# Kernel optimization log

Hardware: AMD Instinct MI355X
Metric: run time of the kernel (lower is better)

The kernel has to match this reference:

```python
import jax, jax.numpy as jnp
import numpy as np

B, A, H, DKEY, NMEM = 1024, 4, 512, 512, 65536
OBS, E1, E2 = 9, 64, 128
DIN = E2 + A + 1  # 133


def _lin_init(k, out_d, in_d):
    s = 1.0 / np.sqrt(in_d)
    kw, kb = jax.random.split(k)
    w = jax.random.uniform(kw, (out_d, in_d), jnp.float32, -s, s)
    b = jax.random.uniform(kb, (out_d,), jnp.float32, -s, s)
    return w, b


def setup_inputs() -> dict:
    key = jax.random.key(0)
    ks = jax.random.split(key, 16)
    inp = {}
    inp["obs"] = jax.random.normal(ks[0], (B, OBS), jnp.float32)
    inp["p_action"] = jax.random.uniform(ks[1], (B, A), jnp.float32)
    inp["p_reward"] = jax.random.normal(ks[2], (B, 1), jnp.float32)
    inp["h0"] = jnp.zeros((1, B, H), jnp.float32)
    inp["c0"] = jnp.zeros((1, B, H), jnp.float32)
    inp["cue"] = jax.random.normal(ks[3], (B, DKEY), jnp.float32)
    # encoder params
    inp["enc_w1"], inp["enc_b1"] = _lin_init(ks[4], E1, OBS)
    inp["enc_w2"], inp["enc_b2"] = _lin_init(ks[5], E2, E1)
    # episodic LSTM params (5 gates: i, f, g, o, r)
    s = 1.0 / np.sqrt(H)
    inp["w_ih"] = jax.random.uniform(ks[6], (5 * H, DIN), jnp.float32, -s, s)
    inp["w_hh"] = jax.random.uniform(ks[7], (5 * H, H), jnp.float32, -s, s)
    inp["b_ih"] = jax.random.uniform(ks[8], (5 * H,), jnp.float32, -s, s)
    inp["b_hh"] = jax.random.uniform(ks[9], (5 * H,), jnp.float32, -s, s)
    # actor / critic heads
    inp["actor_w"], inp["actor_b"] = _lin_init(ks[10], A, H)
    inp["critic_w"], inp["critic_b"] = _lin_init(ks[11], 1, H)
    # DND memory store (keys / values)
    inp["dnd_keys"] = jax.random.normal(ks[12], (NMEM, DKEY), jnp.float32)
    inp["dnd_vals"] = jax.random.normal(ks[13], (NMEM, H), jnp.float32) * 0.1
    return inp


def reference(obs, p_action, p_reward, h0, c0, cue,
              enc_w1, enc_b1, enc_w2, enc_b2,
              w_ih, w_hh, b_ih, b_hh,
              actor_w, actor_b, critic_w, critic_b,
              dnd_keys, dnd_vals):
    # --- encoder MLP ---
    feats = jax.nn.relu(jax.nn.relu(obs @ enc_w1.T + enc_b1) @ enc_w2.T + enc_b2)  # [B, 128]
    x_t = jnp.concatenate([feats, p_action, p_reward], axis=-1)  # [B, DIN]

    # --- DND retrieval: l2 kernel -> softmax-weighted sum of values ---
    d2 = (jnp.sum(cue * cue, axis=-1, keepdims=True)
          - 2.0 * (cue @ dnd_keys.T)
          + jnp.sum(dnd_keys * dnd_keys, axis=-1))  # [B, NMEM]
    sims = -jnp.sqrt(jnp.maximum(d2, 1e-12))
    w = jax.nn.softmax(sims, axis=-1)
    m_t = w @ dnd_vals  # [B, H]

    # --- episodic LSTM step (single timestep) ---
    h, c = h0[0], c0[0]  # [B, H]
    z = x_t @ w_ih.T + h @ w_hh.T + b_ih + b_hh  # [B, 5H]
    i_g = jax.nn.sigmoid(z[:, 0 * H:1 * H])
    f_g = jax.nn.sigmoid(z[:, 1 * H:2 * H])
    g_g = jnp.tanh(z[:, 2 * H:3 * H])
    o_g = jax.nn.sigmoid(z[:, 3 * H:4 * H])
    r_g = jax.nn.sigmoid(z[:, 4 * H:5 * H])  # reinstatement gate for memory
    c_new = f_g * c + i_g * g_g + r_g * m_t
    h_new = o_g * jnp.tanh(c_new)

    # --- heads ---
    action_logits = h_new @ actor_w.T + actor_b  # [B, A]
    value_estimate = h_new @ critic_w.T + critic_b  # [B, 1]
    return action_logits, value_estimate, h_new[None], c_new[None], feats
```

## Files before the change

### kernel.cpp

```cpp
#include <hip/hip_runtime.h>

typedef __bf16 bf16x8 __attribute__((ext_vector_type(8)));
typedef float  f32x4  __attribute__((ext_vector_type(4)));

#define NMEM_   65536
#define NCHUNK_ 16
#define NKC_    (NMEM_/NCHUNK_)
#define XPD_    160

#define WS_KB    ((size_t)0)
#define WS_VT    ((size_t)67108864)
#define WS_KNRM  ((size_t)134217728)
#define WS_QB    ((size_t)134479872)
#define WS_QQ    ((size_t)135528448)
#define WS_OP    ((size_t)135532544)
#define WS_LP    ((size_t)169086976)
#define WS_MT    ((size_t)169152512)
#define WS_XP    ((size_t)171249664)
#define WS_HB    ((size_t)171577344)
#define WS_WIHP  ((size_t)172625920)
#define WS_WHHB  ((size_t)173445120)
#define WS_Z     ((size_t)176066560)

#define OUT_LOG   0
#define OUT_VAL   4096
#define OUT_H     5120
#define OUT_C     529408
#define OUT_FEATS 1053696

__device__ __forceinline__ void gload16(const void* g, void* l) {
    __builtin_amdgcn_global_load_lds(
        (const __attribute__((address_space(1))) void*)g,
        (__attribute__((address_space(3))) void*)l, 16, 0, 0);
}

__global__ __launch_bounds__(256) void enc_kernel(
    const float* __restrict__ obs, const float* __restrict__ pa, const float* __restrict__ pr,
    const float* __restrict__ w1, const float* __restrict__ b1,
    const float* __restrict__ w2, const float* __restrict__ b2,
    float* __restrict__ feats_out, __bf16* __restrict__ xp)
{
    __shared__ float W1s[64*9];
    __shared__ float B1s[64];
    __shared__ float W2s[128*64];
    __shared__ float B2s[128];
    int t = threadIdx.x;
    for (int i = t; i < 64*9;   i += 256) W1s[i] = w1[i];
    for (int i = t; i < 64;     i += 256) B1s[i] = b1[i];
    for (int i = t; i < 128*64; i += 256) W2s[i] = w2[i];
    for (int i = t; i < 128;    i += 256) B2s[i] = b2[i];
    __syncthreads();
    int row = blockIdx.x * 256 + t;
    float ob[9];
    #pragma unroll
    for (int j = 0; j < 9; j++) ob[j] = obs[row*9 + j];
    float h1[64];
    #pragma unroll 4
    for (int i = 0; i < 64; i++) {
        float a = B1s[i];
        #pragma unroll
        for (int j = 0; j < 9; j++) a += ob[j] * W1s[i*9 + j];
        h1[i] = fmaxf(a, 0.f);
    }
    for (int j = 0; j < 128; j += 4) {
        float a0 = B2s[j], a1 = B2s[j+1], a2 = B2s[j+2], a3 = B2s[j+3];
        for (int i = 0; i < 64; i++) {
            float h = h1[i];
            a0 += h * W2s[(j+0)*64 + i];
            a1 += h * W2s[(j+1)*64 + i];
            a2 += h * W2s[(j+2)*64 + i];
            a3 += h * W2s[(j+3)*64 + i];
        }
        a0 = fmaxf(a0,0.f); a1 = fmaxf(a1,0.f); a2 = fmaxf(a2,0.f); a3 = fmaxf(a3,0.f);
        feats_out[row*128 + j+0] = a0; feats_out[row*128 + j+1] = a1;
        feats_out[row*128 + j+2] = a2; feats_out[row*128 + j+3] = a3;
        xp[row*XPD_ + j+0] = (__bf16)a0; xp[row*XPD_ + j+1] = (__bf16)a1;
        xp[row*XPD_ + j+2] = (__bf16)a2; xp[row*XPD_ + j+3] = (__bf16)a3;
    }
    #pragma unroll
    for (int k = 0; k < 4; k++) xp[row*XPD_ + 128 + k] = (__bf16)pa[row*4 + k];
    xp[row*XPD_ + 132] = (__bf16)pr[row];
    #pragma unroll
    for (int c = 133; c < 160; c++) xp[row*XPD_ + c] = (__bf16)0.f;
}

#define CV_KEYS 16384
#define CV_CUE  (CV_KEYS + 256)
#define CV_VT   (CV_CUE + 8192)
#define CM_N1 (2560*512)
#define CM_N2 (1024*512)
#define CM_N3 (2560*160)
#define CV_ALL  (CV_VT + (CM_N1 + CM_N2 + CM_N3 + 255)/256)

__global__ __launch_bounds__(256) void conv_all(
    const float* __restrict__ keys, const float* __restrict__ cue,
    const float* __restrict__ vals,
    const float* __restrict__ whh, const float* __restrict__ h0,
    const float* __restrict__ wih,
    __bf16* __restrict__ Kb, float* __restrict__ knrm,
    __bf16* __restrict__ Qb, float* __restrict__ qq,
    __bf16* __restrict__ Vt,
    __bf16* __restrict__ Whhb, __bf16* __restrict__ Hb, __bf16* __restrict__ Wihp)
{
    int bid = blockIdx.x;
    if (bid < CV_CUE) {
        const float* src; __bf16* dst; float* nrm; int swz, rbase;
        if (bid < CV_KEYS) { src = keys; dst = Kb; nrm = knrm; swz = 1; rbase = bid*4; }
        else               { src = cue;  dst = Qb; nrm = qq;  swz = 0; rbase = (bid-CV_KEYS)*4; }
        int row  = rbase + (threadIdx.x >> 6);
        int lane = threadIdx.x & 63;
        const float* s = src + (size_t)row * 512 + lane * 8;
        float4 v0 = *(const float4*)s;
        float4 v1 = *(const float4*)(s + 4);
        float ss = v0.x*v0.x + v0.y*v0.y + v0.z*v0.z + v0.w*v0.w
                 + v1.x*v1.x + v1.y*v1.y + v1.z*v1.z + v1.w*v1.w;
        bf16x8 o;
        o[0]=(__bf16)v0.x; o[1]=(__bf16)v0.y; o[2]=(__bf16)v0.z; o[3]=(__bf16)v0.w;
        o[4]=(__bf16)v1.x; o[5]=(__bf16)v1.y; o[6]=(__bf16)v1.z; o[7]=(__bf16)v1.w;
        int xorv = swz ? ((row & 15) << 4) : 0;
        *(bf16x8*)((char*)dst + (size_t)row * 1024 + ((lane * 16) ^ xorv)) = o;
        #pragma unroll
        for (int m = 1; m < 64; m <<= 1) ss += __shfl_xor(ss, m, 64);
        if (lane == 0) nrm[row] = ss;
        return;
    }
    if (bid < CV_VT) {
        __shared__ float Ls[64*65];
        int local = bid - CV_CUE;
        int k0 = (local & 1023) * 64, d0 = (local >> 10) * 64;
        int rr = threadIdx.x >> 6, cc = threadIdx.x & 63;
        #pragma unroll
        for (int i = 0; i < 16; i++) {
            int row = i*4 + rr;
            Ls[row*65 + cc] = vals[(size_t)(k0 + row) * 512 + d0 + cc];
        }
        __syncthreads();
        #pragma unroll
        for (int i = 0; i < 16; i++) {
            int drow = i*4 + rr;
            Vt[(size_t)(d0 + drow) * 65536 + k0 + cc] = (__bf16)Ls[cc*65 + drow];
        }
        return;
    }
    {
        int i = (bid - CV_VT) * 256 + threadIdx.x;
        if (i < CM_N1) { Whhb[i] = (__bf16)whh[i]; return; }
        i -= CM_N1;
        if (i < CM_N2) { Hb[i] = (__bf16)h0[i]; return; }
        i -= CM_N2;
        if (i < CM_N3) {
            int r = i / 160, c = i - r * 160;
            Wihp[i] = (c < 133) ? (__bf16)wih[r*133 + c] : (__bf16)0.f;
        }
    }
}

__global__ __launch_bounds__(512) void flash_kernel(
    const __bf16* __restrict__ Kb, const __bf16* __restrict__ Vt,
    const __bf16* __restrict__ Qb, const float* __restrict__ qq,
    const float* __restrict__ knrm,
    float* __restrict__ Opart, float* __restrict__ Lpart)
{
    extern __shared__ char smem[];
    char*   KL = smem;
    __bf16* Pl = (__bf16*)(smem + 131072);
    float*  Lb = (float*) (smem + 149504);

    const int tid = threadIdx.x, lane = tid & 63, w = tid >> 6;
    const int wq = w >> 1, wk = w & 1;
    const int lr = lane & 15, lq = lane >> 4;
    const int chunk = blockIdx.x & 15, qt = blockIdx.x >> 4;
    const int q0 = qt * 64, key0 = chunk * NKC_;

    bf16x8 qA[16];
    #pragma unroll
    for (int ks = 0; ks < 16; ks++)
        qA[ks] = *(const bf16x8*)(Qb + (size_t)(q0 + wq*16 + lr)*512 + ks*32 + lq*8);
    float qq4[4];
    #pragma unroll
    for (int r = 0; r < 4; r++)
        qq4[r] = qq[q0 + wq*16 + lq*4 + r];

    const float*  knp  = knrm + key0 + wk*32 + lr;
    const __bf16* vrow = Vt + (size_t)(w*64 + lr)*65536 + key0 + lq*8;
    const char*   kg   = (const char*)Kb + (size_t)key0 * 1024;

    #pragma unroll
    for (int r = 0; r < 8; ++r)
        gload16(kg + r*8192 + w*1024 + lane*16, KL + r*8192 + w*1024);
    asm volatile("s_waitcnt vmcnt(0)" ::: "memory");
    __builtin_amdgcn_s_barrier();

    f32x4 oacc[4][4] = {};
    float lsum[4] = {};
    int cur = 0;

    #pragma unroll 1
    for (int t = 0; t < 64; ++t) {
        float kn0 = knp[t*64];
        float kn1 = knp[t*64 + 16];
        const __bf16* vb = vrow + ((t + 63) & 63) * 64;
        bf16x8 vf[2][4];
        #pragma unroll
        for (int k2 = 0; k2 < 2; ++k2)
            #pragma unroll
            for (int mf = 0; mf < 4; ++mf)
                vf[k2][mf] = *(const bf16x8*)(vb + k2*32 + (size_t)mf*1048576);
        {
            const char* src = kg + (size_t)((t+1)&63)*65536;
            char* dst = KL + (cur^1)*65536;
            #pragma unroll
            for (int r = 0; r < 8; ++r)
                gload16(src + r*8192 + w*1024 + lane*16, dst + r*8192 + w*1024);
        }
        asm volatile("s_waitcnt vmcnt(18) lgkmcnt(0)" ::: "memory");
        __builtin_amdgcn_sched_barrier(0);
        __builtin_amdgcn_s_barrier();
        const char* kl = KL + cur*65536 + (wk*32 + lr)*1024;
        f32x4 s0 = {0.f,0.f,0.f,0.f}, s1 = {0.f,0.f,0.f,0.f};
        __builtin_amdgcn_s_setprio(1);
        #pragma unroll
        for (int ks = 0; ks < 16; ++ks) {
            int off = (ks*64 + lq*16) ^ (lr << 4);
            bf16x8 kf0 = *(const bf16x8*)(kl + off);
            bf16x8 kf1 = *(const bf16x8*)(kl + 16384 + off);
            s0 = __builtin_amdgcn_mfma_f32_16x16x32_bf16(qA[ks], kf0, s0, 0, 0, 0);
            s1 = __builtin_amdgcn_mfma_f32_16x16x32_bf16(qA[ks], kf1, s1, 0, 0, 0);
        }
        if (t) {
            const char* pr_ = (const char*)Pl + ((t+1)&1)*9216 + lr*144 + lq*16;
            #pragma unroll
            for (int k2 = 0; k2 < 2; ++k2)
                #pragma unroll
                for (int f2 = 0; f2 < 4; ++f2) {
                    bf16x8 pf = *(const bf16x8*)(pr_ + f2*2304 + k2*64);
                    #pragma unroll
                    for (int mf = 0; mf < 4; ++mf)
                        oacc[mf][f2] = __builtin_amdgcn_mfma_f32_16x16x32_bf16(
                            vf[k2][mf], pf, oacc[mf][f2], 0, 0, 0);
                }
        }
        __builtin_amdgcn_s_setprio(0);
        __bf16* Pw = Pl + (t&1)*4608 + wk*32 + lr;
        #pragma unroll
        for (int r = 0; r < 4; ++r) {
            float d20 = fmaxf(qq4[r] + kn0 - 2.f*s0[r], 1e-12f);
            float d21 = fmaxf(qq4[r] + kn1 - 2.f*s1[r], 1e-12f);
            float p0 = __expf(-__builtin_amdgcn_sqrtf(d20));
            float p1 = __expf(-__builtin_amdgcn_sqrtf(d21));
            lsum[r] += p0 + p1;
            Pw[(wq*16 + lq*4 + r)*72]      = (__bf16)p0;
            Pw[(wq*16 + lq*4 + r)*72 + 16] = (__bf16)p1;
        }
        cur ^= 1;
    }

    {
        const __bf16* vb = vrow + 63*64;
        bf16x8 vf[2][4];
        #pragma unroll
        for (int k2 = 0; k2 < 2; ++k2)
            #pragma unroll
            for (int mf = 0; mf < 4; ++mf)
                vf[k2][mf] = *(const bf16x8*)(vb + k2*32 + (size_t)mf*1048576);
        asm volatile("s_waitcnt lgkmcnt(0)" ::: "memory");
        __builtin_amdgcn_sched_barrier(0);
        __builtin_amdgcn_s_barrier();
        const char* pr_ = (const char*)Pl + 9216 + lr*144 + lq*16;
        #pragma unroll
        for (int k2 = 0; k2 < 2; ++k2)
            #pragma unroll
            for (int f2 = 0; f2 < 4; ++f2) {
                bf16x8 pf = *(const bf16x8*)(pr_ + f2*2304 + k2*64);
                #pragma unroll
                for (int mf = 0; mf < 4; ++mf)
                    oacc[mf][f2] = __builtin_amdgcn_mfma_f32_16x16x32_bf16(
                        vf[k2][mf], pf, oacc[mf][f2], 0, 0, 0);
            }
    }
    asm volatile("s_waitcnt vmcnt(0)" ::: "memory");

    const size_t obase = (size_t)((chunk*16 + qt)*512) * 64;
    #pragma unroll
    for (int mf = 0; mf < 4; ++mf)
        #pragma unroll
        for (int f2 = 0; f2 < 4; ++f2)
            #pragma unroll
            for (int r = 0; r < 4; ++r) {
                int d = w*64 + mf*16 + lq*4 + r;
                Opart[obase + (size_t)d*64 + f2*16 + lr] = oacc[mf][f2][r];
            }
    #pragma unroll
    for (int r = 0; r < 4; ++r) {
        float s = lsum[r];
        s += __shfl_xor(s, 1, 64); s += __shfl_xor(s, 2, 64);
        s += __shfl_xor(s, 4, 64); s += __shfl_xor(s, 8, 64);
        if (lr == 0) Lb[(wq*16 + lq*4 + r)*2 + wk] = s;
    }
    __syncthreads();
    if (tid < 64)
        Lpart[chunk*1024 + q0 + tid] = Lb[tid*2] + Lb[tid*2 + 1];
}

__global__ __launch_bounds__(256) void combine_kernel(
    const float* __restrict__ Opart, const float* __restrict__ Lpart,
    float* __restrict__ mt)
{
    __shared__ float Ts[64*65];
    __shared__ float Ls[64];
    int qt = blockIdx.x, db = blockIdx.y * 64, t = threadIdx.x;
    float acc[16] = {};
    for (int c = 0; c < NCHUNK_; c++) {
        size_t base = (size_t)((c*16 + qt)*512 + db) * 64;
        #pragma unroll
        for (int i = 0; i < 16; i++) acc[i] += Opart[base + t + 256*i];
    }
    if (t < 64) {
        float s = 0.f;
        for (int c = 0; c < NCHUNK_; c++) s += Lpart[c*1024 + qt*64 + t];
        Ls[t] = 1.f / s;
    }
    #pragma unroll
    for (int i = 0; i < 16; i++) {
        int idx = t + 256*i;
        Ts[(idx >> 6)*65 + (idx & 63)] = acc[i];
    }
    __syncthreads();
    #pragma unroll
    for (int i = 0; i < 16; i++) {
        int widx = t + 256*i;
        int dloc = widx & 63, ql = widx >> 6;
        mt[(size_t)(qt*64 + ql)*512 + db + dloc] = Ts[dloc*65 + ql] * Ls[ql];
    }
}

__global__ __launch_bounds__(256) void lstm_gemm(
    const __bf16* __restrict__ X,  const __bf16* __restrict__ Wx,
    const __bf16* __restrict__ Hb, const __bf16* __restrict__ Wh,
    const float* __restrict__ bi,  const float* __restrict__ bh,
    float* __restrict__ z)
{
    int tid = threadIdx.x, lane = tid & 63, w = tid >> 6;
    int wr = w >> 1, wc = w & 1;
    int lr = lane & 15, lq = lane >> 4;
    int q0 = blockIdx.x * 64, n0 = blockIdx.y * 64;
    f32x4 acc00 = {}, acc01 = {}, acc10 = {}, acc11 = {};
    #pragma unroll
    for (int ks = 0; ks < 5; ks++) {
        bf16x8 a0 = *(const bf16x8*)(X  + (size_t)(q0 + wr*32      + lr)*XPD_ + ks*32 + lq*8);
        bf16x8 a1 = *(const bf16x8*)(X  + (size_t)(q0 + wr*32 + 16 + lr)*XPD_ + ks*32 + lq*8);
        bf16x8 b0 = *(const bf16x8*)(Wx + (size_t)(n0 + wc*32      + lr)*XPD_ + ks*32 + lq*8);
        bf16x8 b1 = *(const bf16x8*)(Wx + (size_t)(n0 + wc*32 + 16 + lr)*XPD_ + ks*32 + lq*8);
        acc00 = __builtin_amdgcn_mfma_f32_16x16x32_bf16(a0, b0, acc00, 0,0,0);
        acc01 = __builtin_amdgcn_mfma_f32_16x16x32_bf16(a0, b1, acc01, 0,0,0);
        acc10 = __builtin_amdgcn_mfma_f32_16x16x32_bf16(a1, b0, acc10, 0,0,0);
        acc11 = __builtin_amdgcn_mfma_f32_16x16x32_bf16(a1, b1, acc11, 0,0,0);
    }
    #pragma unroll
    for (int ks = 0; ks < 16; ks++) {
        bf16x8 a0 = *(const bf16x8*)(Hb + (size_t)(q0 + wr*32      + lr)*512 + ks*32 + lq*8);
        bf16x8 a1 = *(const bf16x8*)(Hb + (size_t)(q0 + wr*32 + 16 + lr)*512 + ks*32 + lq*8);
        bf16x8 b0 = *(const bf16x8*)(Wh + (size_t)(n0 + wc*32      + lr)*512 + ks*32 + lq*8);
        bf16x8 b1 = *(const bf16x8*)(Wh + (size_t)(n0 + wc*32 + 16 + lr)*512 + ks*32 + lq*8);
        acc00 = __builtin_amdgcn_mfma_f32_16x16x32_bf16(a0, b0, acc00, 0,0,0);
        acc01 = __builtin_amdgcn_mfma_f32_16x16x32_bf16(a0, b1, acc01, 0,0,0);
        acc10 = __builtin_amdgcn_mfma_f32_16x16x32_bf16(a1, b0, acc10, 0,0,0);
        acc11 = __builtin_amdgcn_mfma_f32_16x16x32_bf16(a1, b1, acc11, 0,0,0);
    }
    int nA = n0 + wc*32 + lr, nB = nA + 16;
    float biasA = bi[nA] + bh[nA], biasB = bi[nB] + bh[nB];
    #pragma unroll
    for (int r = 0; r < 4; r++) {
        int qa = q0 + wr*32 + lq*4 + r, qb = qa + 16;
        z[(size_t)qa*2560 + nA] = acc00[r] + biasA;
        z[(size_t)qa*2560 + nB] = acc01[r] + biasB;
        z[(size_t)qb*2560 + nA] = acc10[r] + biasA;
        z[(size_t)qb*2560 + nB] = acc11[r] + biasB;
    }
}

__global__ __launch_bounds__(256) void gates_kernel(
    const float* __restrict__ z,  const float* __restrict__ c0, const float* __restrict__ mt,
    const float* __restrict__ aw, const float* __restrict__ ab,
    const float* __restrict__ cw, const float* __restrict__ cb,
    float* __restrict__ out)
{
    __shared__ float hrow[512];
    __shared__ float red[256];
    int q = blockIdx.x, t = threadIdx.x;
    const float* zq = z + (size_t)q * 2560;
    for (int d = t; d < 512; d += 256) {
        float zi = zq[d], zf = zq[512 + d], zg = zq[1024 + d], zo = zq[1536 + d], zr = zq[2048 + d];
        float ig = 1.f / (1.f + __expf(-zi));
        float fg = 1.f / (1.f + __expf(-zf));
        float gg = tanhf(zg);
        float og = 1.f / (1.f + __expf(-zo));
        float rg = 1.f / (1.f + __expf(-zr));
        float cn = fg * c0[(size_t)q*512 + d] + ig * gg + rg * mt[(size_t)q*512 + d];
        float hn = og * tanhf(cn);
        out[OUT_H + (size_t)q*512 + d] = hn;
        out[OUT_C + (size_t)q*512 + d] = cn;
        hrow[d] = hn;
    }
    __syncthreads();
    for (int o = 0; o < 5; o++) {
        const float* wv = (o < 4) ? (aw + o*512) : cw;
        float p = 0.f;
        for (int d = t; d < 512; d += 256) p += hrow[d] * wv[d];
        red[t] = p;
        __syncthreads();
        for (int s = 128; s > 0; s >>= 1) {
            if (t < s) red[t] += red[t + s];
            __syncthreads();
        }
        if (t == 0) {
            float v = red[0] + ((o < 4) ? ab[o] : cb[0]);
            if (o < 4) out[OUT_LOG + q*4 + o] = v;
            else       out[OUT_VAL + q] = v;
        }
        __syncthreads();
    }
}

extern "C" void kernel_launch(void* const* d_in, const int* in_sizes, int n_in,
                              void* d_out, int out_size, void* d_ws, size_t ws_size,
                              hipStream_t stream) {
    (void)in_sizes; (void)n_in; (void)out_size; (void)ws_size;
    const float* obs   = (const float*)d_in[0];
    const float* pa    = (const float*)d_in[1];
    const float* pr    = (const float*)d_in[2];
    const float* h0    = (const float*)d_in[3];
    const float* c0    = (const float*)d_in[4];
    const float* cue   = (const float*)d_in[5];
    const float* ew1   = (const float*)d_in[6];
    const float* eb1   = (const float*)d_in[7];
    const float* ew2   = (const float*)d_in[8];
    const float* eb2   = (const float*)d_in[9];
    const float* w_ih  = (const float*)d_in[10];
    const float* w_hh  = (const float*)d_in[11];
    const float* b_ih  = (const float*)d_in[12];
    const float* b_hh  = (const float*)d_in[13];
    const float* aw    = (const float*)d_in[14];
    const float* ab    = (const float*)d_in[15];
    const float* cw    = (const float*)d_in[16];
    const float* cb    = (const float*)d_in[17];
    const float* keys  = (const float*)d_in[18];
    const float* vals  = (const float*)d_in[19];

    char* ws = (char*)d_ws;
    __bf16* Kb    = (__bf16*)(ws + WS_KB);
    __bf16* Vt    = (__bf16*)(ws + WS_VT);
    float*  knrm  = (float*) (ws + WS_KNRM);
    __bf16* Qb    = (__bf16*)(ws + WS_QB);
    float*  qq    = (float*) (ws + WS_QQ);
    float*  Opart = (float*) (ws + WS_OP);
    float*  Lpart = (float*) (ws + WS_LP);
    float*  mt    = (float*) (ws + WS_MT);
    __bf16* Xp    = (__bf16*)(ws + WS_XP);
    __bf16* Hb    = (__bf16*)(ws + WS_HB);
    __bf16* Wihp  = (__bf16*)(ws + WS_WIHP);
    __bf16* Whhb  = (__bf16*)(ws + WS_WHHB);
    float*  zbuf  = (float*) (ws + WS_Z);
    float*  out   = (float*)d_out;

    (void)hipFuncSetAttribute((const void*)flash_kernel,
                              hipFuncAttributeMaxDynamicSharedMemorySize, 150528);

    enc_kernel<<<4, 256, 0, stream>>>(obs, pa, pr, ew1, eb1, ew2, eb2, out + OUT_FEATS, Xp);
    conv_all<<<CV_ALL, 256, 0, stream>>>(keys, cue, vals, w_hh, h0, w_ih,
                                         Kb, knrm, Qb, qq, Vt, Whhb, Hb, Wihp);
    flash_kernel<<<256, 512, 150528, stream>>>(Kb, Vt, Qb, qq, knrm, Opart, Lpart);
    combine_kernel<<<dim3(16, 8), 256, 0, stream>>>(Opart, Lpart, mt);
    lstm_gemm<<<dim3(16, 40), 256, 0, stream>>>(Xp, Wihp, Hb, Whhb, b_ih, b_hh, zbuf);
    gates_kernel<<<1024, 256, 0, stream>>>(zbuf, c0, mt, aw, ab, cw, cb, out);
}
```

Measured before the change: 389.7 us.

## Double-buffer V fragments and knorm prefetch, XOR-swizzle P tile in LDS

The flash loop is unrolled by two so V fragments and key norms for the next step are loaded into alternate register sets one iteration ahead, overlapping their global latency with the current step's MFMAs. The padded P tile layout (stride 72 elements) is replaced by a 128-byte-row layout with an XOR swizzle to avoid LDS bank conflicts, which also shrinks dynamic LDS. The cost is a second set of V fragment registers, which raises register pressure in a 512-thread block.

```diff
diff --git a/kernel.cpp b/kernel.cpp
--- a/kernel.cpp
+++ b/kernel.cpp
@@ -162,9 +162,9 @@
     float* __restrict__ Opart, float* __restrict__ Lpart)
 {
     extern __shared__ char smem[];
-    char*   KL = smem;
-    __bf16* Pl = (__bf16*)(smem + 131072);
-    float*  Lb = (float*) (smem + 149504);
+    char*  KL  = smem;
+    char*  Plb = smem + 131072;
+    float* Lb  = (float*)(smem + 147456);
 
     const int tid = threadIdx.x, lane = tid & 63, w = tid >> 6;
     const int wq = w >> 1, wk = w & 1;
@@ -194,88 +194,101 @@
     f32x4 oacc[4][4] = {};
     float lsum[4] = {};
     int cur = 0;
-
-    #pragma unroll 1
-    for (int t = 0; t < 64; ++t) {
-        float kn0 = knp[t*64];
-        float kn1 = knp[t*64 + 16];
-        const __bf16* vb = vrow + ((t + 63) & 63) * 64;
-        bf16x8 vf[2][4];
-        #pragma unroll
-        for (int k2 = 0; k2 < 2; ++k2)
-            #pragma unroll
-            for (int mf = 0; mf < 4; ++mf)
-                vf[k2][mf] = *(const bf16x8*)(vb + k2*32 + (size_t)mf*1048576);
-        {
-            const char* src = kg + (size_t)((t+1)&63)*65536;
-            char* dst = KL + (cur^1)*65536;
-            #pragma unroll
-            for (int r = 0; r < 8; ++r)
-                gload16(src + r*8192 + w*1024 + lane*16, dst + r*8192 + w*1024);
-        }
-        asm volatile("s_waitcnt vmcnt(18) lgkmcnt(0)" ::: "memory");
-        __builtin_amdgcn_sched_barrier(0);
-        __builtin_amdgcn_s_barrier();
-        const char* kl = KL + cur*65536 + (wk*32 + lr)*1024;
-        f32x4 s0 = {0.f,0.f,0.f,0.f}, s1 = {0.f,0.f,0.f,0.f};
-        __builtin_amdgcn_s_setprio(1);
-        #pragma unroll
-        for (int ks = 0; ks < 16; ++ks) {
-            int off = (ks*64 + lq*16) ^ (lr << 4);
-            bf16x8 kf0 = *(const bf16x8*)(kl + off);
-            bf16x8 kf1 = *(const bf16x8*)(kl + 16384 + off);
-            s0 = __builtin_amdgcn_mfma_f32_16x16x32_bf16(qA[ks], kf0, s0, 0, 0, 0);
-            s1 = __builtin_amdgcn_mfma_f32_16x16x32_bf16(qA[ks], kf1, s1, 0, 0, 0);
-        }
-        if (t) {
-            const char* pr_ = (const char*)Pl + ((t+1)&1)*9216 + lr*144 + lq*16;
-            #pragma unroll
-            for (int k2 = 0; k2 < 2; ++k2)
-                #pragma unroll
-                for (int f2 = 0; f2 < 4; ++f2) {
-                    bf16x8 pf = *(const bf16x8*)(pr_ + f2*2304 + k2*64);
-                    #pragma unroll
-                    for (int mf = 0; mf < 4; ++mf)
-                        oacc[mf][f2] = __builtin_amdgcn_mfma_f32_16x16x32_bf16(
-                            vf[k2][mf], pf, oacc[mf][f2], 0, 0, 0);
-                }
-        }
-        __builtin_amdgcn_s_setprio(0);
-        __bf16* Pw = Pl + (t&1)*4608 + wk*32 + lr;
-        #pragma unroll
-        for (int r = 0; r < 4; ++r) {
-            float d20 = fmaxf(qq4[r] + kn0 - 2.f*s0[r], 1e-12f);
-            float d21 = fmaxf(qq4[r] + kn1 - 2.f*s1[r], 1e-12f);
-            float p0 = __expf(-__builtin_amdgcn_sqrtf(d20));
-            float p1 = __expf(-__builtin_amdgcn_sqrtf(d21));
-            lsum[r] += p0 + p1;
-            Pw[(wq*16 + lq*4 + r)*72]      = (__bf16)p0;
-            Pw[(wq*16 + lq*4 + r)*72 + 16] = (__bf16)p1;
-        }
-        cur ^= 1;
-    }
+    bf16x8 vfA[2][4], vfB[2][4];
+    float knA0 = knp[0], knA1 = knp[16], knB0, knB1;
+
+#define FLASH_BODY(T, VC, VN, KC0, KC1, KN0, KN1)                              \
+    {                                                                          \
+        KN0 = knp[(((T)+1)&63)*64];                                            \
+        KN1 = knp[(((T)+1)&63)*64 + 16];                                       \
+        {                              \
+            const char* src_ = kg + (size_t)(((T)+1)&63)*65536;                \
+            char* dst_ = KL + (cur^1)*65536;                                   \
+            _Pragma("unroll")                                                  \
+            for (int r_ = 0; r_ < 8; ++r_)                                     \
+                gload16(src_ + r_*8192 + w*1024 + lane*16,                     \
+                        dst_ + r_*8192 + w*1024);                              \
+        }                                                                      \
+               \
+        asm volatile("s_waitcnt vmcnt(18) lgkmcnt(0)" ::: "memory");           \
+        __builtin_amdgcn_sched_barrier(0);                                     \
+        __builtin_amdgcn_s_barrier();                                          \
+                                     \
+        const char* kl_ = KL + cur*65536 + (wk*32 + lr)*1024;                  \
+        f32x4 s0 = {0.f,0.f,0.f,0.f}, s1 = {0.f,0.f,0.f,0.f};                  \
+        __builtin_amdgcn_s_setprio(1);                                         \
+        _Pragma("unroll")                                                      \
+        for (int ks_ = 0; ks_ < 16; ++ks_) {                                   \
+            int off_ = (ks_*64 + lq*16) ^ (lr << 4);                           \
+            bf16x8 kf0_ = *(const bf16x8*)(kl_ + off_);                        \
+            bf16x8 kf1_ = *(const bf16x8*)(kl_ + 16384 + off_);                \
+            s0 = __builtin_amdgcn_mfma_f32_16x16x32_bf16(qA[ks_], kf0_, s0, 0, 0, 0); \
+            s1 = __builtin_amdgcn_mfma_f32_16x16x32_bf16(qA[ks_], kf1_, s1, 0, 0, 0); \
+        }                                                                      \
+                                \
+        if (T) {                                                               \
+            const char* pb_ = Plb + (((T)+1)&1)*8192;                          \
+            _Pragma("unroll")                                                  \
+            for (int k2_ = 0; k2_ < 2; ++k2_)                                  \
+                _Pragma("unroll")                                              \
+                for (int f2_ = 0; f2_ < 4; ++f2_) {                            \
+                    bf16x8 pf_ = *(const bf16x8*)(pb_ + (f2_*16 + lr)*128      \
+                                 + ((k2_*64 + lq*16) ^ ((lr & 7) << 4)));      \
+                    _Pragma("unroll")                                          \
+                    for (int mf_ = 0; mf_ < 4; ++mf_)                          \
+                        oacc[mf_][f2_] = __builtin_amdgcn_mfma_f32_16x16x32_bf16( \
+                            VC[k2_][mf_], pf_, oacc[mf_][f2_], 0, 0, 0);       \
+                }                                                              \
+        }                                                                      \
+        __builtin_amdgcn_s_setprio(0);                                         \
+                               \
+        {                                                                      \
+            const __bf16* vb_ = vrow + (T)*64;                                 \
+            _Pragma("unroll")                                                  \
+            for (int k2_ = 0; k2_ < 2; ++k2_)                                  \
+                _Pragma("unroll")                                              \
+                for (int mf_ = 0; mf_ < 4; ++mf_)                              \
+                    VN[k2_][mf_] = *(const bf16x8*)(vb_ + k2_*32               \
+                                                    + (size_t)mf_*1048576);    \
+        }                                                                      \
+                \
+        char* pw_ = Plb + ((T)&1)*8192;                                        \
+        _Pragma("unroll")                                                      \
+        for (int r_ = 0; r_ < 4; ++r_) {                                       \
+            float d20_ = fmaxf(qq4[r_] + KC0 - 2.f*s0[r_], 1e-12f);            \
+            float d21_ = fmaxf(qq4[r_] + KC1 - 2.f*s1[r_], 1e-12f);            \
+            float p0_ = __expf(-__builtin_amdgcn_sqrtf(d20_));                 \
+            float p1_ = __expf(-__builtin_amdgcn_sqrtf(d21_));                 \
+            lsum[r_] += p0_ + p1_;                                             \
+            int row_ = wq*16 + lq*4 + r_;                                      \
+            int sw_ = (row_ & 7) << 4;                                         \
+            *(__bf16*)(pw_ + row_*128 + ((((wk*32 + lr)*2)     ) ^ sw_)) = (__bf16)p0_; \
+            *(__bf16*)(pw_ + row_*128 + ((((wk*32 + lr)*2) + 32) ^ sw_)) = (__bf16)p1_; \
+        }                                                                      \
+        cur ^= 1;                                                              \
+    }
+
+    for (int t = 0; t < 64; t += 2) {
+        FLASH_BODY(t,     vfA, vfB, knA0, knA1, knB0, knB1)
+        FLASH_BODY((t+1), vfB, vfA, knB0, knB1, knA0, knA1)
+    }
+#undef FLASH_BODY
 
     {
-        const __bf16* vb = vrow + 63*64;
-        bf16x8 vf[2][4];
-        #pragma unroll
-        for (int k2 = 0; k2 < 2; ++k2)
-            #pragma unroll
-            for (int mf = 0; mf < 4; ++mf)
-                vf[k2][mf] = *(const bf16x8*)(vb + k2*32 + (size_t)mf*1048576);
         asm volatile("s_waitcnt lgkmcnt(0)" ::: "memory");
         __builtin_amdgcn_sched_barrier(0);
         __builtin_amdgcn_s_barrier();
-        const char* pr_ = (const char*)Pl + 9216 + lr*144 + lq*16;
+        const char* pb_ = Plb + 8192;
         #pragma unroll
         for (int k2 = 0; k2 < 2; ++k2)
             #pragma unroll
             for (int f2 = 0; f2 < 4; ++f2) {
-                bf16x8 pf = *(const bf16x8*)(pr_ + f2*2304 + k2*64);
+                bf16x8 pf = *(const bf16x8*)(pb_ + (f2*16 + lr)*128
+                             + ((k2*64 + lq*16) ^ ((lr & 7) << 4)));
                 #pragma unroll
                 for (int mf = 0; mf < 4; ++mf)
                     oacc[mf][f2] = __builtin_amdgcn_mfma_f32_16x16x32_bf16(
-                        vf[k2][mf], pf, oacc[mf][f2], 0, 0, 0);
+                        vfA[k2][mf], pf, oacc[mf][f2], 0, 0, 0);
             }
     }
     asm volatile("s_waitcnt vmcnt(0)" ::: "memory");
@@ -464,12 +477,12 @@
     float*  out   = (float*)d_out;
 
     (void)hipFuncSetAttribute((const void*)flash_kernel,
-                              hipFuncAttributeMaxDynamicSharedMemorySize, 150528);
+                              hipFuncAttributeMaxDynamicSharedMemorySize, 147968);
 
     enc_kernel<<<4, 256, 0, stream>>>(obs, pa, pr, ew1, eb1, ew2, eb2, out + OUT_FEATS, Xp);
     conv_all<<<CV_ALL, 256, 0, stream>>>(keys, cue, vals, w_hh, h0, w_ih,
                                          Kb, knrm, Qb, qq, Vt, Whhb, Hb, Wihp);
-    flash_kernel<<<256, 512, 150528, stream>>>(Kb, Vt, Qb, qq, knrm, Opart, Lpart);
+    flash_kernel<<<256, 512, 147968, stream>>>(Kb, Vt, Qb, qq, knrm, Opart, Lpart);
     combine_kernel<<<dim3(16, 8), 256, 0, stream>>>(Opart, Lpart, mt);
     lstm_gemm<<<dim3(16, 40), 256, 0, stream>>>(Xp, Wihp, Hb, Whhb, b_ih, b_hh, zbuf);
     gates_kernel<<<1024, 256, 0, stream>>>(zbuf, c0, mt, aw, ab, cw, cb, out);
```

Result: slower. 609.7 us (+56.5%).
